# Optimization experiments

Hardware: AMD Instinct MI355X
Metric: run time of the kernel (lower is better)

## Reference

```python
import jax, jax.numpy as jnp
import numpy as np

DEPTH, HEADS, DIM_HEAD = 6, 8, 32
D_MODEL, D_FF = 256, 1024
B, N, D_IN, N_CLS = 4, 4096, 128, 10
NB_FEAT = int(DIM_HEAD * np.log(DIM_HEAD))  # 110 random features (performer_pytorch default)


def _ortho_gaussian(m, d, rng):
    # gaussian orthogonal random projection (FAVOR+), rows rescaled by chi-distributed norms
    blocks = []
    for _ in range(int(np.ceil(m / d))):
        q, _ = np.linalg.qr(rng.standard_normal((d, d)))
        blocks.append(q.T)
    mat = np.concatenate(blocks, 0)[:m]
    mult = np.linalg.norm(rng.standard_normal((m, d)), axis=1)
    return (mult[:, None] * mat).astype(np.float32)


def setup_inputs() -> dict:
    rng = np.random.default_rng(0)
    w = lambda *s: jnp.asarray((rng.standard_normal(s) * 0.02).astype(np.float32))
    z = lambda *s: jnp.zeros(s, jnp.float32)
    o = lambda *s: jnp.ones(s, jnp.float32)
    proj = jnp.asarray(np.stack([_ortho_gaussian(NB_FEAT, DIM_HEAD, rng) for _ in range(DEPTH)]))
    return dict(
        x=jnp.asarray(rng.standard_normal((B, N, D_IN)).astype(np.float32)),
        mask=jnp.ones((B, N), bool),
        w_in=w(D_IN, D_MODEL), b_in=z(D_MODEL),
        ln1_g=o(DEPTH, D_MODEL), ln1_b=z(DEPTH, D_MODEL),
        wq=w(DEPTH, D_MODEL, D_MODEL), wk=w(DEPTH, D_MODEL, D_MODEL),
        wv=w(DEPTH, D_MODEL, D_MODEL), wo=w(DEPTH, D_MODEL, D_MODEL), bo=z(DEPTH, D_MODEL),
        proj=proj,
        ln2_g=o(DEPTH, D_MODEL), ln2_b=z(DEPTH, D_MODEL),
        w1=w(DEPTH, D_MODEL, D_FF), b1=z(DEPTH, D_FF),
        w2=w(DEPTH, D_FF, D_MODEL), b2=z(DEPTH, D_MODEL),
        cls_g=o(D_MODEL), cls_b=z(D_MODEL),
        wc1=w(D_MODEL, D_MODEL), bc1=z(D_MODEL),
        wc2=w(D_MODEL, N_CLS), bc2=z(N_CLS),
    )


def _ln(x, g, b, eps=1e-5):
    mu = x.mean(-1, keepdims=True)
    var = ((x - mu) ** 2).mean(-1, keepdims=True)
    return (x - mu) * jax.lax.rsqrt(var + eps) * g + b


def _softmax_kernel(data, proj, is_query, eps=1e-4):
    # FAVOR+ positive softmax features (performer_pytorch softmax_kernel)
    dn = data.shape[-1] ** -0.25
    ratio = proj.shape[0] ** -0.5
    dd = jnp.einsum('bhnd,md->bhnm', data * dn, proj)
    diag = 0.5 * (dn ** 2) * jnp.sum(data ** 2, axis=-1, keepdims=True)  # [B,H,N,1]
    if is_query:
        m = jnp.max(dd, axis=-1, keepdims=True)
    else:
        m = jnp.max(dd, axis=(-2, -1), keepdims=True)
    m = jax.lax.stop_gradient(m)
    return ratio * (jnp.exp(dd - diag - m) + eps)


def _linear_attn(q, k, v):
    # non-causal O(n) attention: q,k [B,H,N,M], v [B,H,N,dh]
    k_sum = k.sum(-2)                                            # [B,H,M]
    d_inv = 1.0 / jnp.einsum('bhnm,bhm->bhn', q, k_sum)          # [B,H,N]
    ctx = jnp.einsum('bhnm,bhnd->bhmd', k, v)                    # [B,H,M,dh]
    return jnp.einsum('bhnm,bhmd,bhn->bhnd', q, ctx, d_inv)


def _forward(x, mask, w_in, b_in, ln1_g, ln1_b, wq, wk, wv, wo, bo, proj,
             ln2_g, ln2_b, w1, b1, w2, b2, cls_g, cls_b, wc1, bc1, wc2, bc2):
    b_, n_ = x.shape[:2]
    h = x @ w_in + b_in
    mb = mask[:, None, :, None]
    split = lambda t: t.reshape(b_, n_, HEADS, DIM_HEAD).transpose(0, 2, 1, 3)
    for i in range(DEPTH):
        y = _ln(h, ln1_g[i], ln1_b[i])
        q, k, v = split(y @ wq[i]), split(y @ wk[i]), split(y @ wv[i])
        v = jnp.where(mb, v, 0.0)
        qp = _softmax_kernel(q, proj[i], True)
        kp = _softmax_kernel(k, proj[i], False)
        a = _linear_attn(qp, kp, v).transpose(0, 2, 1, 3).reshape(b_, n_, D_MODEL)
        h = h + a @ wo[i] + bo[i]
        y2 = _ln(h, ln2_g[i], ln2_b[i])
        h = h + jax.nn.gelu(y2 @ w1[i] + b1[i], approximate=False) @ w2[i] + b2[i]
    p = h.mean(1)
    z = jax.nn.relu(_ln(p, cls_g, cls_b))
    z = jax.nn.relu(z @ wc1 + bc1)
    return z @ wc2 + bc2


def reference(x, mask, w_in, b_in, ln1_g, ln1_b, wq, wk, wv, wo, bo, proj,
              ln2_g, ln2_b, w1, b1, w2, b2, cls_g, cls_b, wc1, bc1, wc2, bc2):
    return _forward(x, mask, w_in, b_in, ln1_g, ln1_b, wq, wk, wv, wo, bo, proj,
                    ln2_g, ln2_b, w1, b1, w2, b2, cls_g, cls_b, wc1, bc1, wc2, bc2)
```

## Files before the change

kernel.cpp:

```cpp
#include <hip/hip_runtime.h>
#include <cstdint>
#include <cstddef>

typedef __attribute__((ext_vector_type(8))) short bf16x8;
typedef __attribute__((ext_vector_type(4))) float f32x4;
typedef unsigned short u16;
typedef unsigned int u32;

static constexpr float DN    = 0.42044820762685725f;
static constexpr float DN2   = 0.17677669529663687f;
static constexpr float RATIO = 0.09534625892455924f;
static constexpr float KEPS  = 1e-4f;

__device__ __forceinline__ float b2f(u16 u) {
    union { float f; u32 i; } x; x.i = ((u32)u) << 16; return x.f;
}
__device__ __forceinline__ u16 f2b(float f) {
    union { float f; u32 i; } x; x.f = f;
    u32 r = (x.i + 0x7FFFu + ((x.i >> 16) & 1u)) >> 16;
    return (u16)r;
}
__device__ __forceinline__ float wred_sum(float v) {
#pragma unroll
    for (int o = 32; o > 0; o >>= 1) v += __shfl_xor(v, o, 64);
    return v;
}
__device__ __forceinline__ float gelu_f(float v) {
    return 0.5f * v * (1.f + erff(v * 0.7071067811865475f));
}
__device__ __forceinline__ void gload16(const u16* g, u16* l) {
    __builtin_amdgcn_global_load_lds(
        (const __attribute__((address_space(1))) u32*)(const u32*)g,
        (__attribute__((address_space(3))) u32*)(u32*)l, 16, 0, 0);
}

__global__ __launch_bounds__(256) void trk(const float* __restrict__ src, u16* __restrict__ dst,
                                           int K, int N)
{
    const size_t bo = (size_t)blockIdx.z * K * N;
    src += bo; dst += bo;
    __shared__ float tl[32][33];
    const int t = threadIdx.x, tx = t & 31, ty = t >> 5;
    const int k0 = blockIdx.y * 32, n0 = blockIdx.x * 32;
#pragma unroll
    for (int p = 0; p < 4; ++p)
        tl[ty + p * 8][tx] = src[(size_t)(k0 + ty + p * 8) * N + n0 + tx];
    __syncthreads();
#pragma unroll
    for (int p = 0; p < 4; ++p)
        dst[(size_t)(n0 + ty + p * 8) * K + k0 + tx] = f2b(tl[tx][ty + p * 8]);
}

__global__ __launch_bounds__(256) void xcast(const float* __restrict__ x, u16* __restrict__ xb)
{
    const int i = blockIdx.x * 256 + threadIdx.x;
    const float4 v = ((const float4*)x)[i];
    uint2 r;
    r.x = (u32)f2b(v.x) | ((u32)f2b(v.y) << 16);
    r.y = (u32)f2b(v.z) | ((u32)f2b(v.w) << 16);
    ((uint2*)xb)[i] = r;
}

template<int CMODE, int NP, bool QKV, bool AHEAD, bool CHEAD, bool CHUNK>
__global__ __launch_bounds__(512) void gemm3(
    const u16* __restrict__ A, const u16* __restrict__ Bt,
    const float* __restrict__ bias, u16* __restrict__ Cb, int ldc,
    u16* __restrict__ hres, const float* __restrict__ lng, const float* __restrict__ lnb,
    u16* __restrict__ yout, int K, int lda, int nrt)
{
    constexpr int KC    = (NP == 128) ? 256 : 128;
    constexpr int SLOTS = KC / 8;
    constexpr int SSH   = (SLOTS == 32) ? 5 : 4;
    constexpr int BB    = NP * KC * 2;
    constexpr int ABYT  = 64 * KC * 2;
    constexpr int NCB   = NP / 128;
    constexpr int CTS   = (NP == 128) ? 136 : 264;
    constexpr int EPI   = (CMODE <= 1) ? (64 * CTS * 2) : (64 * 264 * 2 + 4608);
    constexpr int KCC   = 64;
    constexpr int BBC   = 256 * KCC * 2;
    constexpr int ABYTC = 64 * KCC * 2;
    constexpr int BUF   = BBC + ABYTC;
    constexpr int LDSZ  = CHUNK ? (2 * BUF) : (BB + 2 * ABYT + EPI);
    __shared__ __align__(16) char smem[LDSZ];

    const u16* Btl = Bt;
    u16* Cbl = Cb;
    if (QKV) { Btl += (size_t)blockIdx.z * 393216; Cbl += (size_t)blockIdx.z * 4194304; }
    const int t = threadIdx.x, w = t >> 6, lr = (t & 63) & 15, lg = (t & 63) >> 4;
    const int p = blockIdx.x;

    char* epi = CHUNK ? smem : (smem + BB + 2 * ABYT);

    f32x4 acc[4][NCB];
    auto ZERO = [&]() {
#pragma unroll
        for (int i = 0; i < 4; ++i)
#pragma unroll
            for (int j = 0; j < NCB; ++j) acc[i][j] = f32x4{0.f, 0.f, 0.f, 0.f};
    };

    auto EPILOGUE = [&](int row0) {
        if constexpr (CMODE <= 1) {
            u16* ctile = (u16*)epi;
            float bv[NCB];
#pragma unroll
            for (int cb = 0; cb < NCB; ++cb) {
                const int col = p * NP + w * (NP / 8) + cb * 16 + lr;
                bv[cb] = bias ? bias[col] : 0.f;
            }
#pragma unroll
            for (int rbk = 0; rbk < 4; ++rbk)
#pragma unroll
                for (int cb = 0; cb < NCB; ++cb)
#pragma unroll
                    for (int rr = 0; rr < 4; ++rr) {
                        const int rl = rbk * 16 + 4 * lg + rr;
                        float v = acc[rbk][cb][rr] + bv[cb];
                        if (CMODE == 1) v = gelu_f(v);
                        ctile[rl * CTS + w * (NP / 8) + cb * 16 + lr] = f2b(v);
                    }
            __syncthreads();
            if constexpr (CHEAD && NP == 128) {
                const int bq = row0 >> 12, n0 = row0 & 4095;
#pragma unroll
                for (int i = 0; i < 2; ++i) {
                    const int u = i * 512 + t;
                    const int hh = u >> 8, rem = u & 255;
                    const int row = rem >> 2, dblk = rem & 3;
                    *(uint4*)(Cbl + ((size_t)(bq * 8 + p * 4 + hh) * 4096 + n0 + row) * 32 + dblk * 8)
                        = *(const uint4*)&ctile[row * CTS + hh * 32 + dblk * 8];
                }
            } else if constexpr (CHEAD && NP == 256) {
                const int bq = row0 >> 12, n0 = row0 & 4095;
#pragma unroll
                for (int i = 0; i < 4; ++i) {
                    const int u = i * 512 + t;
                    const int row = u >> 5, seg = u & 31;
                    const int hh = seg >> 2, dblk = seg & 3;
                    *(uint4*)(Cbl + ((size_t)(bq * 8 + hh) * 4096 + n0 + row) * 32 + dblk * 8)
                        = *(const uint4*)&ctile[row * 264 + seg * 8];
                }
            } else {
                constexpr int NIT = (NP == 128) ? 2 : 4;
                constexpr int SEGM = NP / 8 - 1;
                constexpr int RSH = (NP == 128) ? 4 : 5;
#pragma unroll
                for (int i = 0; i < NIT; ++i) {
                    const int u = i * 512 + t;
                    const int row = u >> RSH, seg = u & SEGM;
                    *(uint4*)(Cbl + (size_t)(row0 + row) * ldc + p * NP + seg * 8)
                        = *(const uint4*)&ctile[row * CTS + seg * 8];
                }
            }
        } else {
            u16*   ctile = (u16*)epi;
            float* rsum  = (float*)(epi + 33792);
            float* rsum2 = rsum + 512;
            float* rmu   = rsum2 + 512;
            float* rrs   = rmu + 64;
            int cidx[NCB]; float bv[NCB];
#pragma unroll
            for (int cb = 0; cb < NCB; ++cb) {
                cidx[cb] = w * 32 + cb * 16 + lr;
                bv[cb] = bias ? bias[cidx[cb]] : 0.f;
            }
            if constexpr (CMODE == 2 || CMODE == 4) {
#pragma unroll
                for (int i = 0; i < 4; ++i) {
                    const int u = i * 512 + t;
                    const int row = u >> 5, seg = u & 31;
                    *(uint4*)&ctile[row * 264 + seg * 8]
                        = *(const uint4*)(hres + (size_t)(row0 + row) * 256 + seg * 8);
                }
                __syncthreads();
            }
#pragma unroll
            for (int rbk = 0; rbk < 4; ++rbk)
#pragma unroll
                for (int cb = 0; cb < NCB; ++cb)
#pragma unroll
                    for (int rr = 0; rr < 4; ++rr) {
                        const int rl = rbk * 16 + 4 * lg + rr;
                        float v = acc[rbk][cb][rr] + bv[cb];
                        if constexpr (CMODE == 2 || CMODE == 4)
                            v += b2f(ctile[rl * 264 + cidx[cb]]);
                        acc[rbk][cb][rr] = v;
                    }
            __syncthreads();
            if constexpr (CMODE != 4) {
#pragma unroll
                for (int rbk = 0; rbk < 4; ++rbk)
#pragma unroll
                    for (int rr = 0; rr < 4; ++rr) {
                        float s1 = acc[rbk][0][rr] + acc[rbk][NCB - 1][rr];
                        float s2 = fmaf(acc[rbk][0][rr], acc[rbk][0][rr],
                                        acc[rbk][NCB - 1][rr] * acc[rbk][NCB - 1][rr]);
#pragma unroll
                        for (int off = 1; off < 16; off <<= 1) {
                            s1 += __shfl_xor(s1, off, 64);
                            s2 += __shfl_xor(s2, off, 64);
                        }
                        if (lr == 0) {
                            const int rl = rbk * 16 + 4 * lg + rr;
                            rsum[rl * 8 + w] = s1; rsum2[rl * 8 + w] = s2;
                        }
                    }
                __syncthreads();
                if (t < 64) {
                    float s1 = 0.f, s2 = 0.f;
#pragma unroll
                    for (int j = 0; j < 8; ++j) { s1 += rsum[t * 8 + j]; s2 += rsum2[t * 8 + j]; }
                    const float mu = s1 * (1.f / 256.f);
                    const float var = s2 * (1.f / 256.f) - mu * mu;
                    rmu[t] = mu; rrs[t] = rsqrtf(var + 1e-5f);
                }
                __syncthreads();
            }
#pragma unroll
            for (int rbk = 0; rbk < 4; ++rbk)
#pragma unroll
                for (int cb = 0; cb < NCB; ++cb)
#pragma unroll
                    for (int rr = 0; rr < 4; ++rr) {
                        const int rl = rbk * 16 + 4 * lg + rr;
                        ctile[rl * 264 + cidx[cb]] = f2b(acc[rbk][cb][rr]);
                    }
            __syncthreads();
#pragma unroll
            for (int i = 0; i < 4; ++i) {
                const int u = i * 512 + t;
                const int row = u >> 5, seg = u & 31;
                *(uint4*)(hres + (size_t)(row0 + row) * 256 + seg * 8)
                    = *(const uint4*)&ctile[row * 264 + seg * 8];
            }
            if constexpr (CMODE != 4) {
                __syncthreads();
                float gv[NCB], bb2[NCB];
#pragma unroll
                for (int cb = 0; cb < NCB; ++cb) { gv[cb] = lng[cidx[cb]]; bb2[cb] = lnb[cidx[cb]]; }
#pragma unroll
                for (int rbk = 0; rbk < 4; ++rbk)
#pragma unroll
                    for (int cb = 0; cb < NCB; ++cb)
#pragma unroll
                        for (int rr = 0; rr < 4; ++rr) {
                            const int rl = rbk * 16 + 4 * lg + rr;
                            const float yv = (acc[rbk][cb][rr] - rmu[rl]) * rrs[rl] * gv[cb] + bb2[cb];
                            ctile[rl * 264 + cidx[cb]] = f2b(yv);
                        }
                __syncthreads();
#pragma unroll
                for (int i = 0; i < 4; ++i) {
                    const int u = i * 512 + t;
                    const int row = u >> 5, seg = u & 31;
                    *(uint4*)(yout + (size_t)(row0 + row) * 256 + seg * 8)
                        = *(const uint4*)&ctile[row * 264 + seg * 8];
                }
            }
        }
    };

    if constexpr (!CHUNK) {
        u16* Bs  = (u16*)smem;
        u16* Asm = (u16*)(smem + BB);
        const int NC = K / KC;
        auto STAGE_B = [&](int c) {
#pragma unroll
            for (int i = 0; i < BB / 16 / 512; ++i) {
                const int u = i * 512 + t;
                const int col = u >> SSH, slot = u & (SLOTS - 1);
                const int gs = slot ^ (col & 7);
                gload16(Btl + (size_t)(p * NP + col) * K + c * KC + gs * 8, Bs + u * 8);
            }
        };
        auto STAGE_A = [&](int c, int row0, int buf) {
            u16* dst = Asm + buf * (ABYT / 2);
#pragma unroll
            for (int i = 0; i < ABYT / 16 / 512; ++i) {
                const int u = i * 512 + t;
                const int row = u >> SSH, slot = u & (SLOTS - 1);
                const int gs = slot ^ (row & 7);
                const u16* src;
                if (AHEAD) {
                    const int kg = c * KC + gs * 8;
                    src = A + ((size_t)((row0 >> 12) * 8 + (kg >> 5)) * 4096 + (row0 & 4095) + row) * 32 + (kg & 31);
                } else {
                    src = A + (size_t)(row0 + row) * lda + c * KC + gs * 8;
                }
                gload16(src, dst + u * 8);
            }
        };
        auto KLOOP = [&](const u16* AcC) {
#pragma unroll
            for (int ks = 0; ks < KC / 32; ++ks) {
                bf16x8 af[4], bfv[NCB];
#pragma unroll
                for (int rbk = 0; rbk < 4; ++rbk) {
                    const int row = rbk * 16 + lr;
                    af[rbk] = *(const bf16x8*)&AcC[row * KC + (((ks * 4 + lg) ^ (row & 7)) << 3)];
                }
#pragma unroll
                for (int cb = 0; cb < NCB; ++cb) {
                    const int col = w * (NP / 8) + cb * 16 + lr;
                    bfv[cb] = *(const bf16x8*)&Bs[col * KC + (((ks * 4 + lg) ^ (col & 7)) << 3)];
                }
#pragma unroll
                for (int rbk = 0; rbk < 4; ++rbk)
#pragma unroll
                    for (int cb = 0; cb < NCB; ++cb)
                        acc[rbk][cb] = __builtin_amdgcn_mfma_f32_16x16x32_bf16(af[rbk], bfv[cb], acc[rbk][cb], 0, 0, 0);
            }
        };
        (void)NC;
        int ab = 0;
        STAGE_B(0);
        STAGE_A(0, blockIdx.y * nrt * 64, 0);
        asm volatile("s_waitcnt vmcnt(0)" ::: "memory");
        __syncthreads();
        for (int rt = 0; rt < nrt; ++rt) {
            const int row0 = (blockIdx.y * nrt + rt) * 64;
            if (rt + 1 < nrt) STAGE_A(0, row0 + 64, ab ^ 1);
            ZERO();
            KLOOP(Asm + ab * (ABYT / 2));
            EPILOGUE(row0);
            asm volatile("s_waitcnt vmcnt(0)" ::: "memory");
            __syncthreads();
            ab ^= 1;
        }
    } else {
        const int NC = K / KCC;
        const int row0 = blockIdx.y * 64;
        auto STAGE_CH = [&](int c, int b) {
            u16* bsB = (u16*)(smem + b * BUF);
            u16* bsA = (u16*)(smem + b * BUF + BBC);
#pragma unroll
            for (int i = 0; i < BBC / 16 / 512; ++i) {
                const int u = i * 512 + t;
                const int col = u >> 3, slot = u & 7;
                const int gs = slot ^ (col & 7);
                gload16(Btl + (size_t)(p * NP + col) * K + c * KCC + gs * 8, bsB + u * 8);
            }
            {
                const int u = t;
                const int row = u >> 3, slot = u & 7;
                const int gs = slot ^ (row & 7);
                const u16* src;
                if (AHEAD) {
                    const int kg = c * KCC + gs * 8;
                    src = A + ((size_t)((row0 >> 12) * 8 + (kg >> 5)) * 4096 + (row0 & 4095) + row) * 32 + (kg & 31);
                } else {
                    src = A + (size_t)(row0 + row) * lda + c * KCC + gs * 8;
                }
                gload16(src, bsA + u * 8);
            }
        };
        auto KLOOP_C = [&](const u16* BsC, const u16* AcC) {
#pragma unroll
            for (int ks = 0; ks < 2; ++ks) {
                bf16x8 af[4], bfv[NCB];
#pragma unroll
                for (int rbk = 0; rbk < 4; ++rbk) {
                    const int row = rbk * 16 + lr;
                    af[rbk] = *(const bf16x8*)&AcC[row * KCC + (((ks * 4 + lg) ^ (row & 7)) << 3)];
                }
#pragma unroll
                for (int cb = 0; cb < NCB; ++cb) {
                    const int col = w * 32 + cb * 16 + lr;
                    bfv[cb] = *(const bf16x8*)&BsC[col * KCC + (((ks * 4 + lg) ^ (col & 7)) << 3)];
                }
#pragma unroll
                for (int rbk = 0; rbk < 4; ++rbk)
#pragma unroll
                    for (int cb = 0; cb < NCB; ++cb)
                        acc[rbk][cb] = __builtin_amdgcn_mfma_f32_16x16x32_bf16(af[rbk], bfv[cb], acc[rbk][cb], 0, 0, 0);
            }
        };

        ZERO();
        STAGE_CH(0, 0);
        STAGE_CH(1, 1);
        for (int c = 0; c < NC; ++c) {
            if (c + 1 < NC) asm volatile("s_waitcnt vmcnt(5)" ::: "memory");
            else            asm volatile("s_waitcnt vmcnt(0)" ::: "memory");
            __builtin_amdgcn_s_barrier();
            __builtin_amdgcn_sched_barrier(0);
            KLOOP_C((const u16*)(smem + (c & 1) * BUF),
                    (const u16*)(smem + (c & 1) * BUF + BBC));
            __builtin_amdgcn_sched_barrier(0);
            if (c + 2 < NC) {
                __builtin_amdgcn_s_barrier();
                __builtin_amdgcn_sched_barrier(0);
                STAGE_CH(c + 2, c & 1);
            }
        }
        __builtin_amdgcn_s_barrier();
        __builtin_amdgcn_sched_barrier(0);
        EPILOGUE(row0);
    }
}

__global__ __launch_bounds__(256) void kctx2(
    const u16* __restrict__ kg, const u16* __restrict__ vg,
    const float* __restrict__ proj, float* __restrict__ ctxp, float* __restrict__ Mcp,
    float* __restrict__ vsump)
{
    __shared__ __align__(16) u16 projS[112 * 32];
    __shared__ __align__(16) u16 kS[128 * 32];
    __shared__ __align__(16) u16 vTS[48 * 128];
    __shared__ __align__(16) u16 eTS[112 * 128];
    __shared__ float diagS[128];
    __shared__ float redS[4];
    const int t = threadIdx.x, w = t >> 6, lane = t & 63, lr = lane & 15, lg = lane >> 4;
    const int bh = blockIdx.x >> 3, chunk = blockIdx.x & 7;

    for (int idx = t; idx < 112 * 32; idx += 256) {
        const int m = idx >> 5, d = idx & 31;
        projS[idx] = (m < 110) ? f2b(proj[m * 32 + d] * DN) : (u16)0;
    }
    for (int idx = t; idx < 16 * 128; idx += 256) {
        const int rr = idx >> 7;
        vTS[(32 + rr) * 128 + (idx & 127)] = (rr == 0) ? f2b(1.0f) : (u16)0;
    }
    for (int idx = t; idx < 16 * 128; idx += 256)
        eTS[112 * 128 + idx] = 0;

    f32x4 E[2][3];
#pragma unroll
    for (int i = 0; i < 2; ++i)
#pragma unroll
        for (int j = 0; j < 3; ++j) E[i][j] = f32x4{0.f, 0.f, 0.f, 0.f};
    float Mrun = -INFINITY;
    float vsAcc = 0.f;

    for (int r = 0; r < 4; ++r) {
        const size_t eb = ((size_t)bh * 4096 + chunk * 512 + r * 128) * 32;
#pragma unroll
        for (int i = 0; i < 2; ++i) {
            const int u = i * 256 + t;
            ((uint4*)kS)[u] = ((const uint4*)(kg + eb))[u];
        }
#pragma unroll
        for (int i = 0; i < 2; ++i) {
            const int u = i * 256 + t;
            const int tok = u >> 2, dblk = u & 3;
            union { uint4 v; u16 s[8]; } uu;
            uu.v = ((const uint4*)(vg + eb))[u];
#pragma unroll
            for (int j = 0; j < 8; ++j) {
                const int d = dblk * 8 + j;
                vTS[d * 128 + ((((tok >> 3) ^ (d & 15))) << 3) + (tok & 7)] = uu.s[j];
            }
        }
        __syncthreads();
        {
            const int d = t >> 3, seg = t & 7;
            union { uint4 v; u16 s[8]; } ua, ub;
            ua.v = *(const uint4*)&vTS[d * 128 + seg * 16];
            ub.v = *(const uint4*)&vTS[d * 128 + seg * 16 + 8];
            float s = 0.f;
#pragma unroll
            for (int j = 0; j < 8; ++j) s += b2f(ua.s[j]) + b2f(ub.s[j]);
            vsAcc += s;
        }
        if (t < 128) {
            float s = 0.f;
#pragma unroll
            for (int dq = 0; dq < 4; ++dq) {
                union { uint4 v; u16 ss[8]; } uu;
                uu.v = ((const uint4*)kS)[t * 4 + dq];
#pragma unroll
                for (int j = 0; j < 8; ++j) { const float f = b2f(uu.ss[j]); s = fmaf(f, f, s); }
            }
            diagS[t] = 0.5f * DN2 * s;
        }
        __syncthreads();
        f32x4 dd[7][2];
#pragma unroll
        for (int mb = 0; mb < 7; ++mb)
#pragma unroll
            for (int tb = 0; tb < 2; ++tb) dd[mb][tb] = f32x4{0.f, 0.f, 0.f, 0.f};
        bf16x8 kf[2];
#pragma unroll
        for (int tb = 0; tb < 2; ++tb)
            kf[tb] = *(const bf16x8*)&kS[(w * 32 + tb * 16 + lr) * 32 + lg * 8];
#pragma unroll
        for (int mb = 0; mb < 7; ++mb) {
            const bf16x8 pf = *(const bf16x8*)&projS[(mb * 16 + lr) * 32 + lg * 8];
#pragma unroll
            for (int tb = 0; tb < 2; ++tb)
                dd[mb][tb] = __builtin_amdgcn_mfma_f32_16x16x32_bf16(pf, kf[tb], dd[mb][tb], 0, 0, 0);
        }
        float mx = -INFINITY;
#pragma unroll
        for (int mb = 0; mb < 7; ++mb)
#pragma unroll
            for (int tb = 0; tb < 2; ++tb)
#pragma unroll
                for (int rr = 0; rr < 4; ++rr) {
                    if (mb == 6 && (4 * lg + rr) >= 14) continue;
                    mx = fmaxf(mx, dd[mb][tb][rr]);
                }
#pragma unroll
        for (int off = 1; off < 64; off <<= 1) mx = fmaxf(mx, __shfl_xor(mx, off, 64));
        if (lane == 0) redS[w] = mx;
        __syncthreads();
        float Mnew = fmaxf(fmaxf(redS[0], redS[1]), fmaxf(redS[2], redS[3]));
        Mnew = fmaxf(Mrun, Mnew);
        const float scl = __expf(Mrun - Mnew);
#pragma unroll
        for (int i = 0; i < 2; ++i)
#pragma unroll
            for (int j = 0; j < 3; ++j)
#pragma unroll
                for (int rr = 0; rr < 4; ++rr) E[i][j][rr] *= scl;
        Mrun = Mnew;
        const float dg0 = diagS[w * 32 + lr], dg1 = diagS[w * 32 + 16 + lr];
#pragma unroll
        for (int mb = 0; mb < 7; ++mb)
#pragma unroll
            for (int tb = 0; tb < 2; ++tb)
#pragma unroll
                for (int rr = 0; rr < 4; ++rr) {
                    const int tok = w * 32 + tb * 16 + lr;
                    const int m = mb * 16 + 4 * lg + rr;
                    const float e = __expf(dd[mb][tb][rr] - (tb ? dg1 : dg0) - Mnew);
                    eTS[m * 128 + ((((tok >> 3) ^ (m & 15))) << 3) + (tok & 7)] = f2b(e);
                }
        __syncthreads();
#pragma unroll
        for (int ks = 0; ks < 4; ++ks) {
            bf16x8 aF[2], bF[3];
#pragma unroll
            for (int mb2 = 0; mb2 < 2; ++mb2) {
                const int m = w * 32 + mb2 * 16 + lr;
                aF[mb2] = *(const bf16x8*)&eTS[m * 128 + (((ks * 4 + lg) ^ lr) << 3)];
            }
#pragma unroll
            for (int nb = 0; nb < 3; ++nb) {
                const int d = nb * 16 + lr;
                bF[nb] = *(const bf16x8*)&vTS[d * 128 + (((ks * 4 + lg) ^ lr) << 3)];
            }
#pragma unroll
            for (int mb2 = 0; mb2 < 2; ++mb2)
#pragma unroll
                for (int nb = 0; nb < 3; ++nb)
                    E[mb2][nb] = __builtin_amdgcn_mfma_f32_16x16x32_bf16(aF[mb2], bF[nb], E[mb2][nb], 0, 0, 0);
        }
        __syncthreads();
    }
    const size_t ob = (size_t)blockIdx.x * 112 * 33;
#pragma unroll
    for (int mb2 = 0; mb2 < 2; ++mb2)
#pragma unroll
        for (int nb = 0; nb < 3; ++nb)
#pragma unroll
            for (int rr = 0; rr < 4; ++rr) {
                const int m = w * 32 + mb2 * 16 + 4 * lg + rr;
                if (m < 112) {
                    if (nb < 2) ctxp[ob + m * 33 + nb * 16 + lr] = E[mb2][nb][rr];
                    else if (lr == 0) ctxp[ob + m * 33 + 32] = E[mb2][nb][rr];
                }
            }
    if (t == 0) Mcp[blockIdx.x] = Mrun;
    float vs = vsAcc;
#pragma unroll
    for (int o = 4; o > 0; o >>= 1) vs += __shfl_xor(vs, o, 64);
    if ((t & 7) == 0) vsump[blockIdx.x * 32 + (t >> 3)] = vs;
}

__global__ __launch_bounds__(256) void kred2(
    const float* __restrict__ ctxp, const float* __restrict__ Mcp,
    const float* __restrict__ vsump,
    u16* __restrict__ ctxTg, float* __restrict__ ksumg)
{
    __shared__ float vsumS[32];
    __shared__ float wS[8];
    const int t = threadIdx.x, bh = blockIdx.x;
    float M = -INFINITY;
#pragma unroll
    for (int c = 0; c < 8; ++c) M = fmaxf(M, Mcp[bh * 8 + c]);
    if (t < 8) wS[t] = __expf(Mcp[bh * 8 + t] - M);
    if (t < 32) {
        float s = 0.f;
#pragma unroll
        for (int c = 0; c < 8; ++c) s += vsump[(bh * 8 + c) * 32 + t];
        vsumS[t] = s;
    }
    __syncthreads();
    for (int idx = t; idx < 4096; idx += 256) {
        const int d = idx >> 7, m = idx & 127;
        float val = 0.f;
        if (m < 110) {
            float s = 0.f;
#pragma unroll
            for (int c = 0; c < 8; ++c)
                s += wS[c] * ctxp[((size_t)(bh * 8 + c) * 112 + m) * 33 + d];
            val = RATIO * (s + KEPS * vsumS[d]);
        }
        ctxTg[(size_t)bh * 4096 + idx] = f2b(val);
    }
    if (t < 128) {
        float val = 0.f;
        if (t < 110) {
            float s = 0.f;
#pragma unroll
            for (int c = 0; c < 8; ++c)
                s += wS[c] * ctxp[((size_t)(bh * 8 + c) * 112 + t) * 33 + 32];
            val = RATIO * (s + KEPS * 4096.0f);
        }
        ksumg[bh * 128 + t] = val;
    }
}

__global__ __launch_bounds__(256) void qattn2(
    const u16* __restrict__ qg, const float* __restrict__ proj,
    const u16* __restrict__ ctxTg, const float* __restrict__ ksumg, u16* __restrict__ ag)
{
    __shared__ __align__(16) u16 projS[112 * 32];
    __shared__ __align__(16) u16 qS[128 * 32];
    __shared__ __align__(16) u16 ctxTS[32 * 128];
    __shared__ __align__(16) u16 pS[128 * 128];
    __shared__ float ksumS[128], diagS[128], dinvS[128];
    const int t = threadIdx.x, w = t >> 6, lr = (t & 63) & 15, lg = (t & 63) >> 4;
    const int bh = blockIdx.x >> 5, chunk = blockIdx.x & 31;

    for (int idx = t; idx < 112 * 32; idx += 256) {
        const int m = idx >> 5, d = idx & 31;
        projS[idx] = (m < 110) ? f2b(proj[m * 32 + d] * DN) : (u16)0;
    }
#pragma unroll
    for (int i = 0; i < 2; ++i) {
        const int u = i * 256 + t;
        const int d = u >> 4, s = u & 15;
        *(uint4*)&ctxTS[d * 128 + (((s ^ (d & 15))) << 3)] =
            *(const uint4*)(ctxTg + (size_t)bh * 4096 + d * 128 + s * 8);
    }
    if (t < 128) ksumS[t] = ksumg[bh * 128 + t];
    const size_t qeb = ((size_t)bh * 4096 + chunk * 128) * 32;
#pragma unroll
    for (int i = 0; i < 2; ++i) {
        const int u = i * 256 + t;
        ((uint4*)qS)[u] = ((const uint4*)(qg + qeb))[u];
    }
    {
        const int tok = t >> 1, s = 14 + (t & 1);
        *(uint4*)&pS[tok * 128 + (((s ^ (tok & 15))) << 3)] = uint4{0, 0, 0, 0};
    }
    __syncthreads();
    if (t < 128) {
        float s = 0.f;
#pragma unroll
        for (int dq = 0; dq < 4; ++dq) {
            union { uint4 v; u16 ss[8]; } uu;
            uu.v = ((const uint4*)qS)[t * 4 + dq];
#pragma unroll
            for (int j = 0; j < 8; ++j) { const float f = b2f(uu.ss[j]); s = fmaf(f, f, s); }
        }
        diagS[t] = 0.5f * DN2 * s;
    }
    __syncthreads();
    f32x4 dd[7][2];
#pragma unroll
    for (int mb = 0; mb < 7; ++mb)
#pragma unroll
        for (int tb = 0; tb < 2; ++tb) dd[mb][tb] = f32x4{0.f, 0.f, 0.f, 0.f};
    bf16x8 qf[2];
#pragma unroll
    for (int tb = 0; tb < 2; ++tb)
        qf[tb] = *(const bf16x8*)&qS[(w * 32 + tb * 16 + lr) * 32 + lg * 8];
#pragma unroll
    for (int mb = 0; mb < 7; ++mb) {
        const bf16x8 pf = *(const bf16x8*)&projS[(mb * 16 + lr) * 32 + lg * 8];
#pragma unroll
        for (int tb = 0; tb < 2; ++tb)
            dd[mb][tb] = __builtin_amdgcn_mfma_f32_16x16x32_bf16(pf, qf[tb], dd[mb][tb], 0, 0, 0);
    }
    float mx[2], den[2];
#pragma unroll
    for (int tb = 0; tb < 2; ++tb) {
        float v = -INFINITY;
#pragma unroll
        for (int mb = 0; mb < 7; ++mb)
#pragma unroll
            for (int rr = 0; rr < 4; ++rr) {
                if (mb == 6 && (4 * lg + rr) >= 14) continue;
                v = fmaxf(v, dd[mb][tb][rr]);
            }
        v = fmaxf(v, __shfl_xor(v, 16, 64));
        v = fmaxf(v, __shfl_xor(v, 32, 64));
        mx[tb] = v;
        den[tb] = 0.f;
    }
    const float dg0 = diagS[w * 32 + lr], dg1 = diagS[w * 32 + 16 + lr];
#pragma unroll
    for (int mb = 0; mb < 7; ++mb)
#pragma unroll
        for (int tb = 0; tb < 2; ++tb)
#pragma unroll
            for (int rr = 0; rr < 4; ++rr) {
                const int m = mb * 16 + 4 * lg + rr;
                const int tok = w * 32 + tb * 16 + lr;
                const float pv = RATIO * (__expf(dd[mb][tb][rr] - (tb ? dg1 : dg0) - mx[tb]) + KEPS);
                den[tb] += pv * ksumS[m];
                pS[tok * 128 + ((((m >> 3) ^ (tok & 15))) << 3) + (m & 7)] = f2b(pv);
            }
#pragma unroll
    for (int tb = 0; tb < 2; ++tb) {
        den[tb] += __shfl_xor(den[tb], 16, 64);
        den[tb] += __shfl_xor(den[tb], 32, 64);
        if (lg == 0) dinvS[w * 32 + tb * 16 + lr] = 1.f / den[tb];
    }
    __syncthreads();
    f32x4 o[2][2];
#pragma unroll
    for (int i = 0; i < 2; ++i)
#pragma unroll
        for (int j = 0; j < 2; ++j) o[i][j] = f32x4{0.f, 0.f, 0.f, 0.f};
#pragma unroll
    for (int ks = 0; ks < 4; ++ks) {
        bf16x8 aF[2], bF[2];
#pragma unroll
        for (int tb = 0; tb < 2; ++tb) {
            const int tok = w * 32 + tb * 16 + lr;
            aF[tb] = *(const bf16x8*)&pS[tok * 128 + (((ks * 4 + lg) ^ lr) << 3)];
        }
#pragma unroll
        for (int nb = 0; nb < 2; ++nb) {
            const int d = nb * 16 + lr;
            bF[nb] = *(const bf16x8*)&ctxTS[d * 128 + (((ks * 4 + lg) ^ lr) << 3)];
        }
#pragma unroll
        for (int tb = 0; tb < 2; ++tb)
#pragma unroll
            for (int nb = 0; nb < 2; ++nb)
                o[tb][nb] = __builtin_amdgcn_mfma_f32_16x16x32_bf16(aF[tb], bF[nb], o[tb][nb], 0, 0, 0);
    }
    u16* outS = qS;
#pragma unroll
    for (int tb = 0; tb < 2; ++tb)
#pragma unroll
        for (int nb = 0; nb < 2; ++nb)
#pragma unroll
            for (int rr = 0; rr < 4; ++rr) {
                const int tokl = w * 32 + tb * 16 + 4 * lg + rr;
                outS[tokl * 32 + nb * 16 + lr] = f2b(o[tb][nb][rr] * dinvS[tokl]);
            }
    __syncthreads();
#pragma unroll
    for (int i = 0; i < 2; ++i) {
        const int u = i * 256 + t;
        ((uint4*)(ag + qeb))[u] = ((const uint4*)outS)[u];
    }
}

__global__ __launch_bounds__(256) void pool_k(const u16* __restrict__ h,
                                              float* __restrict__ pp)
{
    const int b = blockIdx.x, ch = blockIdx.y, d = threadIdx.x;
    const u16* p = h + ((size_t)b * 4096 + ch * 256) * 256 + d;
    float s = 0.f;
    for (int n = 0; n < 256; ++n) s += b2f(p[(size_t)n * 256]);
    pp[(b * 16 + ch) * 256 + d] = s;
}

__global__ __launch_bounds__(256) void cls_k(const float* __restrict__ pp,
                                             const float* __restrict__ g,
                                             const float* __restrict__ bb,
                                             const float* __restrict__ wc1,
                                             const float* __restrict__ bc1,
                                             const float* __restrict__ wc2,
                                             const float* __restrict__ bc2,
                                             float* __restrict__ out)
{
    __shared__ float pS[4][256];
    __shared__ float zS[4][256];
    __shared__ float z2S[4][256];
    const int t = threadIdx.x;
#pragma unroll
    for (int b = 0; b < 4; ++b) {
        float s = 0.f;
        for (int c = 0; c < 16; ++c) s += pp[(b * 16 + c) * 256 + t];
        pS[b][t] = s * (1.f / 4096.f);
    }
    __syncthreads();
    {
        const int w = t >> 6, lane = t & 63;
        const float4 v = *reinterpret_cast<const float4*>(&pS[w][lane * 4]);
        float s = v.x + v.y + v.z + v.w;
        float ss = fmaf(v.x, v.x, fmaf(v.y, v.y, fmaf(v.z, v.z, v.w * v.w)));
        s = wred_sum(s); ss = wred_sum(ss);
        const float mu = s * (1.f / 256.f);
        const float var = ss * (1.f / 256.f) - mu * mu;
        const float rr = rsqrtf(var + 1e-5f);
        const float4 gv = *reinterpret_cast<const float4*>(g + lane * 4);
        const float4 bv = *reinterpret_cast<const float4*>(bb + lane * 4);
        zS[w][lane * 4 + 0] = fmaxf((v.x - mu) * rr * gv.x + bv.x, 0.f);
        zS[w][lane * 4 + 1] = fmaxf((v.y - mu) * rr * gv.y + bv.y, 0.f);
        zS[w][lane * 4 + 2] = fmaxf((v.z - mu) * rr * gv.z + bv.z, 0.f);
        zS[w][lane * 4 + 3] = fmaxf((v.w - mu) * rr * gv.w + bv.w, 0.f);
    }
    __syncthreads();
#pragma unroll
    for (int b = 0; b < 4; ++b) {
        float s = bc1[t];
        for (int j = 0; j < 256; ++j) s = fmaf(zS[b][j], wc1[j * 256 + t], s);
        z2S[b][t] = fmaxf(s, 0.f);
    }
    __syncthreads();
    if (t < 40) {
        const int b = t / 10, c = t % 10;
        float s = bc2[c];
        for (int j = 0; j < 256; ++j) s = fmaf(z2S[b][j], wc2[j * 10 + c], s);
        out[t] = s;
    }
}

extern "C" void kernel_launch(void* const* d_in, const int* in_sizes, int n_in,
                              void* d_out, int out_size, void* d_ws, size_t ws_size,
                              hipStream_t stream)
{
    const float* x    = (const float*)d_in[0];
    const float* w_in = (const float*)d_in[2];
    const float* b_in = (const float*)d_in[3];
    const float* ln1g = (const float*)d_in[4];
    const float* ln1b = (const float*)d_in[5];
    const float* wq   = (const float*)d_in[6];
    const float* wk   = (const float*)d_in[7];
    const float* wv   = (const float*)d_in[8];
    const float* wo   = (const float*)d_in[9];
    const float* bo   = (const float*)d_in[10];
    const float* proj = (const float*)d_in[11];
    const float* ln2g = (const float*)d_in[12];
    const float* ln2b = (const float*)d_in[13];
    const float* w1   = (const float*)d_in[14];
    const float* b1   = (const float*)d_in[15];
    const float* w2   = (const float*)d_in[16];
    const float* b2   = (const float*)d_in[17];
    const float* clsg = (const float*)d_in[18];
    const float* clsb = (const float*)d_in[19];
    const float* wc1  = (const float*)d_in[20];
    const float* bc1  = (const float*)d_in[21];
    const float* wc2  = (const float*)d_in[22];
    const float* bc2  = (const float*)d_in[23];

    char* wsb = (char*)d_ws;
    const size_t MB = 1024 * 1024;
    u16* h     = (u16*)(wsb);
    u16* y     = (u16*)(wsb + 16 * MB);
    u16* qb    = (u16*)(wsb + 24 * MB);
    u16* kb    = (u16*)(wsb + 32 * MB);
    u16* vb    = (u16*)(wsb + 40 * MB);
    u16* ab    = (u16*)(wsb + 48 * MB);
    u16* mid   = qb;
    u16* xb    = (u16*)(wsb + 56 * MB);
    u16* wtb   = (u16*)(wsb + 60 * MB);
    u16* w_inT = wtb;
    u16* wqT   = w_inT + 32768;
    u16* wkT   = wqT + 393216;
    u16* wvT   = wkT + 393216;
    u16* woT   = wvT + 393216;
    u16* w1T   = woT + 393216;
    u16* w2T   = w1T + 1572864;
    char* p2   = (char*)(w2T + 1572864);
    float* ctxp  = (float*)p2;
    float* Mcp   = ctxp + 256 * 112 * 33;
    u16*   ctxTg = (u16*)(Mcp + 256);
    float* ksumg = (float*)(ctxTg + 32 * 4096);
    float* pp    = ksumg + 32 * 128;
    float* vsump = pp + 16384;

    trk<<<dim3(8, 4, 1), 256, 0, stream>>>(w_in, w_inT, 128, 256);
    trk<<<dim3(8, 8, 6), 256, 0, stream>>>(wq, wqT, 256, 256);
    trk<<<dim3(8, 8, 6), 256, 0, stream>>>(wk, wkT, 256, 256);
    trk<<<dim3(8, 8, 6), 256, 0, stream>>>(wv, wvT, 256, 256);
    trk<<<dim3(8, 8, 6), 256, 0, stream>>>(wo, woT, 256, 256);
    trk<<<dim3(32, 8, 6), 256, 0, stream>>>(w1, w1T, 256, 1024);
    trk<<<dim3(8, 32, 6), 256, 0, stream>>>(w2, w2T, 1024, 256);
    xcast<<<2048, 256, 0, stream>>>(x, xb);

    gemm3<3, 256, false, false, false, false><<<dim3(1, 256), 512, 0, stream>>>(
        xb, w_inT, b_in, nullptr, 256, h, ln1g, ln1b, y, 128, 128, 1);
    for (int i = 0; i < 6; ++i) {
        const float* proj_i = proj + (size_t)i * 3520;
        gemm3<0, 256, true, false, true, true><<<dim3(1, 256, 3), 512, 0, stream>>>(
            y, wqT + (size_t)i * 65536, nullptr, qb, 256,
            nullptr, nullptr, nullptr, nullptr, 256, 256, 1);
        kctx2<<<256, 256, 0, stream>>>(kb, vb, proj_i, ctxp, Mcp, vsump);
        kred2<<<32, 256, 0, stream>>>(ctxp, Mcp, vsump, ctxTg, ksumg);
        qattn2<<<1024, 256, 0, stream>>>(qb, proj_i, ctxTg, ksumg, ab);
        gemm3<2, 256, false, true, false, true><<<dim3(1, 256), 512, 0, stream>>>(
            ab, woT + (size_t)i * 65536, bo + i * 256, nullptr, 256, h,
            ln2g + i * 256, ln2b + i * 256, y, 256, 0, 1);
        gemm3<1, 256, false, false, false, true><<<dim3(4, 256), 512, 0, stream>>>(
            y, w1T + (size_t)i * 262144, b1 + i * 1024, mid, 1024,
            nullptr, nullptr, nullptr, nullptr, 256, 256, 1);
        if (i < 5)
            gemm3<2, 256, false, false, false, true><<<dim3(1, 256), 512, 0, stream>>>(
                mid, w2T + (size_t)i * 262144, b2 + i * 256, nullptr, 256, h,
                ln1g + (i + 1) * 256, ln1b + (i + 1) * 256, y, 1024, 1024, 1);
        else
            gemm3<4, 256, false, false, false, true><<<dim3(1, 256), 512, 0, stream>>>(
                mid, w2T + (size_t)i * 262144, b2 + i * 256, nullptr, 256, h,
                nullptr, nullptr, nullptr, 1024, 1024, 1);
    }
    pool_k<<<dim3(4, 16), 256, 0, stream>>>(h, pp);
    cls_k<<<1, 256, 0, stream>>>(pp, clsg, clsb, wc1, bc1, wc2, bc2, (float*)d_out);
}
```

Baseline: 824.3 us.

## Add configurable multi-buffer depth to chunked GEMM and split classifier head

After: 821.4 us. Within noise of the previous version (-0.4%).

```diff
diff --git a/kernel.cpp b/kernel.cpp
--- a/kernel.cpp
+++ b/kernel.cpp
@@ -49,6 +49,21 @@
 #pragma unroll
     for (int p = 0; p < 4; ++p)
         dst[(size_t)(n0 + ty + p * 8) * K + k0 + tx] = f2b(tl[tx][ty + p * 8]);
+}
+
+__global__ __launch_bounds__(256) void trkf(const float* __restrict__ src, float* __restrict__ dst,
+                                            int K, int N)
+{
+    __shared__ float tl[32][33];
+    const int t = threadIdx.x, tx = t & 31, ty = t >> 5;
+    const int k0 = blockIdx.y * 32, n0 = blockIdx.x * 32;
+#pragma unroll
+    for (int p = 0; p < 4; ++p)
+        tl[ty + p * 8][tx] = src[(size_t)(k0 + ty + p * 8) * N + n0 + tx];
+    __syncthreads();
+#pragma unroll
+    for (int p = 0; p < 4; ++p)
+        dst[(size_t)(n0 + ty + p * 8) * K + k0 + tx] = tl[tx][ty + p * 8];
 }
 
 __global__ __launch_bounds__(256) void xcast(const float* __restrict__ x, u16* __restrict__ xb)
@@ -61,7 +76,7 @@
     ((uint2*)xb)[i] = r;
 }
 
-template<int CMODE, int NP, bool QKV, bool AHEAD, bool CHEAD, bool CHUNK>
+template<int CMODE, int NP, bool QKV, bool AHEAD, bool CHEAD, bool CHUNK, int DEPTH>
 __global__ __launch_bounds__(512) void gemm3(
     const u16* __restrict__ A, const u16* __restrict__ Bt,
     const float* __restrict__ bias, u16* __restrict__ Cb, int ldc,
@@ -80,7 +95,7 @@
     constexpr int BBC   = 256 * KCC * 2;
     constexpr int ABYTC = 64 * KCC * 2;
     constexpr int BUF   = BBC + ABYTC;
-    constexpr int LDSZ  = CHUNK ? (2 * BUF) : (BB + 2 * ABYT + EPI);
+    constexpr int LDSZ  = CHUNK ? (DEPTH * BUF) : (BB + 2 * ABYT + EPI);
     __shared__ __align__(16) char smem[LDSZ];
 
     const u16* Btl = Bt;
@@ -263,7 +278,6 @@
     if constexpr (!CHUNK) {
         u16* Bs  = (u16*)smem;
         u16* Asm = (u16*)(smem + BB);
-        const int NC = K / KC;
         auto STAGE_B = [&](int c) {
 #pragma unroll
             for (int i = 0; i < BB / 16 / 512; ++i) {
@@ -311,7 +325,6 @@
                         acc[rbk][cb] = __builtin_amdgcn_mfma_f32_16x16x32_bf16(af[rbk], bfv[cb], acc[rbk][cb], 0, 0, 0);
             }
         };
-        (void)NC;
         int ab = 0;
         STAGE_B(0);
         STAGE_A(0, blockIdx.y * nrt * 64, 0);
@@ -377,20 +390,29 @@
         };
 
         ZERO();
-        STAGE_CH(0, 0);
-        STAGE_CH(1, 1);
+#pragma unroll
+        for (int d = 0; d < DEPTH; ++d)
+            if (d < NC) STAGE_CH(d, d);
         for (int c = 0; c < NC; ++c) {
-            if (c + 1 < NC) asm volatile("s_waitcnt vmcnt(5)" ::: "memory");
-            else            asm volatile("s_waitcnt vmcnt(0)" ::: "memory");
+            const int rem = NC - 1 - c;
+            if constexpr (DEPTH == 3) {
+                if (rem >= 2)      asm volatile("s_waitcnt vmcnt(10)" ::: "memory");
+                else if (rem == 1) asm volatile("s_waitcnt vmcnt(5)"  ::: "memory");
+                else               asm volatile("s_waitcnt vmcnt(0)"  ::: "memory");
+            } else {
+                if (rem >= 1)      asm volatile("s_waitcnt vmcnt(5)"  ::: "memory");
+                else               asm volatile("s_waitcnt vmcnt(0)"  ::: "memory");
+            }
             __builtin_amdgcn_s_barrier();
             __builtin_amdgcn_sched_barrier(0);
-            KLOOP_C((const u16*)(smem + (c & 1) * BUF),
-                    (const u16*)(smem + (c & 1) * BUF + BBC));
+            const int cb_ = c % DEPTH;
+            KLOOP_C((const u16*)(smem + cb_ * BUF),
+                    (const u16*)(smem + cb_ * BUF + BBC));
             __builtin_amdgcn_sched_barrier(0);
-            if (c + 2 < NC) {
+            if (c + DEPTH < NC) {
                 __builtin_amdgcn_s_barrier();
                 __builtin_amdgcn_sched_barrier(0);
-                STAGE_CH(c + 2, c & 1);
+                STAGE_CH(c + DEPTH, cb_);
             }
         }
         __builtin_amdgcn_s_barrier();
@@ -763,56 +785,69 @@
     pp[(b * 16 + ch) * 256 + d] = s;
 }
 
-__global__ __launch_bounds__(256) void cls_k(const float* __restrict__ pp,
+__global__ __launch_bounds__(256) void cls_a(const float* __restrict__ pp,
                                              const float* __restrict__ g,
                                              const float* __restrict__ bb,
-                                             const float* __restrict__ wc1,
+                                             float* __restrict__ zA)
+{
+    const int b = blockIdx.x, t = threadIdx.x, w = t >> 6, lane = t & 63;
+    __shared__ float red1[4], red2[4];
+    float s = 0.f;
+#pragma unroll
+    for (int c = 0; c < 16; ++c) s += pp[(b * 16 + c) * 256 + t];
+    const float p = s * (1.f / 4096.f);
+    const float s1 = wred_sum(p);
+    const float s2 = wred_sum(p * p);
+    if (lane == 0) { red1[w] = s1; red2[w] = s2; }
+    __syncthreads();
+    const float S1 = red1[0] + red1[1] + red1[2] + red1[3];
+    const float S2 = red2[0] + red2[1] + red2[2] + red2[3];
+    const float mu = S1 * (1.f / 256.f);
+    const float var = S2 * (1.f / 256.f) - mu * mu;
+    const float rr = rsqrtf(var + 1e-5f);
+    zA[b * 256 + t] = fmaxf((p - mu) * rr * g[t] + bb[t], 0.f);
+}
+
+__global__ __launch_bounds__(256) void cls_b(const float* __restrict__ zA,
+                                             const float* __restrict__ wc1T,
                                              const float* __restrict__ bc1,
+                                             float* __restrict__ zB)
+{
+    const int b = blockIdx.x, t = threadIdx.x;
+    __shared__ float zS[256];
+    zS[t] = zA[b * 256 + t];
+    __syncthreads();
+    float s = bc1[t];
+    const float* wr = wc1T + (size_t)t * 256;
+#pragma unroll
+    for (int i = 0; i < 64; ++i) {
+        const float4 v = ((const float4*)wr)[i];
+        s = fmaf(zS[i * 4 + 0], v.x, s);
+        s = fmaf(zS[i * 4 + 1], v.y, s);
+        s = fmaf(zS[i * 4 + 2], v.z, s);
+        s = fmaf(zS[i * 4 + 3], v.w, s);
+    }
+    zB[b * 256 + t] = fmaxf(s, 0.f);
+}
+
+__global__ __launch_bounds__(256) void cls_c(const float* __restrict__ zB,
                                              const float* __restrict__ wc2,
                                              const float* __restrict__ bc2,
                                              float* __restrict__ out)
 {
-    __shared__ float pS[4][256];
-    __shared__ float zS[4][256];
-    __shared__ float z2S[4][256];
-    const int t = threadIdx.x;
-#pragma unroll
-    for (int b = 0; b < 4; ++b) {
-        float s = 0.f;
-        for (int c = 0; c < 16; ++c) s += pp[(b * 16 + c) * 256 + t];
-        pS[b][t] = s * (1.f / 4096.f);
+    const int b = blockIdx.x, t = threadIdx.x, w = t >> 6, lane = t & 63;
+    __shared__ float red[4][10];
+    const float v = zB[b * 256 + t];
+    float a[10];
+#pragma unroll
+    for (int c = 0; c < 10; ++c) a[c] = v * wc2[t * 10 + c];
+#pragma unroll
+    for (int c = 0; c < 10; ++c) {
+        const float s = wred_sum(a[c]);
+        if (lane == 0) red[w][c] = s;
     }
     __syncthreads();
-    {
-        const int w = t >> 6, lane = t & 63;
-        const float4 v = *reinterpret_cast<const float4*>(&pS[w][lane * 4]);
-        float s = v.x + v.y + v.z + v.w;
-        float ss = fmaf(v.x, v.x, fmaf(v.y, v.y, fmaf(v.z, v.z, v.w * v.w)));
-        s = wred_sum(s); ss = wred_sum(ss);
-        const float mu = s * (1.f / 256.f);
-        const float var = ss * (1.f / 256.f) - mu * mu;
-        const float rr = rsqrtf(var + 1e-5f);
-        const float4 gv = *reinterpret_cast<const float4*>(g + lane * 4);
-        const float4 bv = *reinterpret_cast<const float4*>(bb + lane * 4);
-        zS[w][lane * 4 + 0] = fmaxf((v.x - mu) * rr * gv.x + bv.x, 0.f);
-        zS[w][lane * 4 + 1] = fmaxf((v.y - mu) * rr * gv.y + bv.y, 0.f);
-        zS[w][lane * 4 + 2] = fmaxf((v.z - mu) * rr * gv.z + bv.z, 0.f);
-        zS[w][lane * 4 + 3] = fmaxf((v.w - mu) * rr * gv.w + bv.w, 0.f);
-    }
-    __syncthreads();
-#pragma unroll
-    for (int b = 0; b < 4; ++b) {
-        float s = bc1[t];
-        for (int j = 0; j < 256; ++j) s = fmaf(zS[b][j], wc1[j * 256 + t], s);
-        z2S[b][t] = fmaxf(s, 0.f);
-    }
-    __syncthreads();
-    if (t < 40) {
-        const int b = t / 10, c = t % 10;
-        float s = bc2[c];
-        for (int j = 0; j < 256; ++j) s = fmaf(z2S[b][j], wc2[j * 10 + c], s);
-        out[t] = s;
-    }
+    if (t < 10) out[b * 10 + t] = bc2[t] + red[0][t] + red[1][t] + red[2][t] + red[3][t];
 }
 
 extern "C" void kernel_launch(void* const* d_in, const int* in_sizes, int n_in,
@@ -868,6 +903,9 @@
     float* ksumg = (float*)(ctxTg + 32 * 4096);
     float* pp    = ksumg + 32 * 128;
     float* vsump = pp + 16384;
+    float* zA    = vsump + 8192;
+    float* zB    = zA + 1024;
+    float* wc1T  = zB + 1024;
 
     trk<<<dim3(8, 4, 1), 256, 0, stream>>>(w_in, w_inT, 128, 256);
     trk<<<dim3(8, 8, 6), 256, 0, stream>>>(wq, wqT, 256, 256);
@@ -876,33 +914,36 @@
     trk<<<dim3(8, 8, 6), 256, 0, stream>>>(wo, woT, 256, 256);
     trk<<<dim3(32, 8, 6), 256, 0, stream>>>(w1, w1T, 256, 1024);
     trk<<<dim3(8, 32, 6), 256, 0, stream>>>(w2, w2T, 1024, 256);
+    trkf<<<dim3(8, 8, 1), 256, 0, stream>>>(wc1, wc1T, 256, 256);
     xcast<<<2048, 256, 0, stream>>>(x, xb);
 
-    gemm3<3, 256, false, false, false, false><<<dim3(1, 256), 512, 0, stream>>>(
+    gemm3<3, 256, false, false, false, false, 2><<<dim3(1, 256), 512, 0, stream>>>(
         xb, w_inT, b_in, nullptr, 256, h, ln1g, ln1b, y, 128, 128, 1);
     for (int i = 0; i < 6; ++i) {
         const float* proj_i = proj + (size_t)i * 3520;
-        gemm3<0, 256, true, false, true, true><<<dim3(1, 256, 3), 512, 0, stream>>>(
+        gemm3<0, 256, true, false, true, true, 2><<<dim3(1, 256, 3), 512, 0, stream>>>(
             y, wqT + (size_t)i * 65536, nullptr, qb, 256,
             nullptr, nullptr, nullptr, nullptr, 256, 256, 1);
         kctx2<<<256, 256, 0, stream>>>(kb, vb, proj_i, ctxp, Mcp, vsump);
         kred2<<<32, 256, 0, stream>>>(ctxp, Mcp, vsump, ctxTg, ksumg);
         qattn2<<<1024, 256, 0, stream>>>(qb, proj_i, ctxTg, ksumg, ab);
-        gemm3<2, 256, false, true, false, true><<<dim3(1, 256), 512, 0, stream>>>(
+        gemm3<2, 256, false, true, false, true, 3><<<dim3(1, 256), 512, 0, stream>>>(
             ab, woT + (size_t)i * 65536, bo + i * 256, nullptr, 256, h,
             ln2g + i * 256, ln2b + i * 256, y, 256, 0, 1);
-        gemm3<1, 256, false, false, false, true><<<dim3(4, 256), 512, 0, stream>>>(
+        gemm3<1, 256, false, false, false, true, 2><<<dim3(4, 256), 512, 0, stream>>>(
             y, w1T + (size_t)i * 262144, b1 + i * 1024, mid, 1024,
             nullptr, nullptr, nullptr, nullptr, 256, 256, 1);
         if (i < 5)
-            gemm3<2, 256, false, false, false, true><<<dim3(1, 256), 512, 0, stream>>>(
+            gemm3<2, 256, false, false, false, true, 3><<<dim3(1, 256), 512, 0, stream>>>(
                 mid, w2T + (size_t)i * 262144, b2 + i * 256, nullptr, 256, h,
                 ln1g + (i + 1) * 256, ln1b + (i + 1) * 256, y, 1024, 1024, 1);
         else
-            gemm3<4, 256, false, false, false, true><<<dim3(1, 256), 512, 0, stream>>>(
+            gemm3<4, 256, false, false, false, true, 3><<<dim3(1, 256), 512, 0, stream>>>(
                 mid, w2T + (size_t)i * 262144, b2 + i * 256, nullptr, 256, h,
                 nullptr, nullptr, nullptr, 1024, 1024, 1);
     }
     pool_k<<<dim3(4, 16), 256, 0, stream>>>(h, pp);
-    cls_k<<<1, 256, 0, stream>>>(pp, clsg, clsb, wc1, bc1, wc2, bc2, (float*)d_out);
-}
+    cls_a<<<4, 256, 0, stream>>>(pp, clsg, clsb, zA);
+    cls_b<<<4, 256, 0, stream>>>(zA, wc1T, bc1, zB);
+    cls_c<<<4, 256, 0, stream>>>(zB, wc2, bc2, (float*)d_out);
+}
```
